# Optimization experiments

Measured on AMD Instinct MI355X. Metric: run time of the kernel, lower is better.

The kernel has to match this reference:

```python
import jax, jax.numpy as jnp
import numpy as np

H, D = 16, 64          # num_heads, head_dim
OUT = H * D            # out_dim = 1024
W1, W2 = 32, 32        # sliding windows
EPS_NORM = 1e-7
EPS_LN = 1e-5


def setup_inputs() -> dict:
    key = jax.random.key(0)
    ks = jax.random.split(key, 6)
    B, S, IN = 2, 2048, 1024
    x = jax.random.normal(ks[0], (B, S, IN), dtype=jnp.float32)
    scale = 0.02
    W_Q = jax.random.normal(ks[1], (IN, OUT), dtype=jnp.float32) * scale
    W_K = jax.random.normal(ks[2], (IN, OUT), dtype=jnp.float32) * scale
    W_V = jax.random.normal(ks[3], (IN, OUT), dtype=jnp.float32) * scale
    W_Kp = jax.random.normal(ks[4], (IN, OUT), dtype=jnp.float32) * scale
    W_O = jax.random.normal(ks[5], (OUT, OUT), dtype=jnp.float32) * scale
    ln_gamma = jnp.ones((OUT,), dtype=jnp.float32)
    ln_beta = jnp.zeros((OUT,), dtype=jnp.float32)
    return {"x": x, "W_Q": W_Q, "W_K": W_K, "W_V": W_V, "W_Kp": W_Kp,
            "W_O": W_O, "ln_gamma": ln_gamma, "ln_beta": ln_beta}


def _l2norm(t):
    return t / (jnp.linalg.norm(t, axis=-1, keepdims=True) + EPS_NORM)


def reference(x, W_Q, W_K, W_V, W_Kp, W_O, ln_gamma, ln_beta):
    B, S, _ = x.shape
    # projections -> (B, S, H, D)
    Q = _l2norm((x @ W_Q).reshape(B, S, H, D))
    K = _l2norm((x @ W_K).reshape(B, S, H, D))
    Kp = _l2norm((x @ W_Kp).reshape(B, S, H, D))
    V = (x @ W_V).reshape(B, S, H, D)
    # windowed keys/values (last w1/w2 positions, as in the PyTorch fallback)
    K_win = K[:, -W1:]
    Kp_win = Kp[:, -W2:]
    V_win = V[:, -W1:]
    Vp_win = V[:, -W2:]
    # triple product A_ijk = q.k.k' / sqrt(D) -> (B, S, H, w1, w2)
    A = jnp.einsum('bshd,bjhd,bkhd->bshjk', Q, K_win, Kp_win) / jnp.sqrt(jnp.float32(D))
    # causal window mask: allow j <= i + w1 - S and k <= i + w2 - S
    s_idx = jnp.arange(S)[:, None, None]
    j_idx = jnp.arange(W1)[None, :, None]
    k_idx = jnp.arange(W2)[None, None, :]
    mask = (j_idx > s_idx + (W1 - S)) | (k_idx > s_idx + (W2 - S))  # (S, w1, w2)
    neg_inf = jnp.float32(-jnp.inf)
    A = jnp.where(mask[None, :, None, :, :], neg_inf, A)
    # joint softmax over (j, k); fully-masked query rows produce zeros
    A_flat = A.reshape(B, S, H, W1 * W2)
    all_masked = jnp.all(A_flat == neg_inf, axis=-1, keepdims=True)
    A_safe = jnp.where(all_masked, 0.0, A_flat)
    P = jax.nn.softmax(A_safe, axis=-1)
    P = jnp.where(all_masked, 0.0, P).reshape(B, S, H, W1, W2)
    # value outer-product weighting (V' = V)
    Z = jnp.einsum('bshjk,bjhd,bkhd->bshd', P, V_win, Vp_win)
    out = Z.reshape(B, S, OUT) @ W_O
    out = out + x  # residual (shapes match)
    # LayerNorm
    mu = jnp.mean(out, axis=-1, keepdims=True)
    var = jnp.mean((out - mu) ** 2, axis=-1, keepdims=True)
    out = (out - mu) / jnp.sqrt(var + EPS_LN) * ln_gamma + ln_beta
    return out
```

## Files before the change

kernel.cpp:

```cpp
#include <hip/hip_runtime.h>
#include <math.h>


#define XS 68
#define WS 68
#define PS 36

#define YP_STR   262144
#define NKS_P    4
#define DP_OFF   (NKS_P * YP_STR)
#define DP_STR   65536

__device__ __forceinline__ void ln_row(
    const float4* __restrict__ x4, const float4* __restrict__ g4,
    const float4* __restrict__ b4, float4* __restrict__ out4,
    int row, int lane) {
  float4 v[4];
  #pragma unroll
  for (int i = 0; i < 4; i++) v[i] = x4[row * 256 + i * 64 + lane];
  float sum = 0.f, ss = 0.f;
  #pragma unroll
  for (int i = 0; i < 4; i++) {
    sum += v[i].x + v[i].y + v[i].z + v[i].w;
    ss  += v[i].x * v[i].x + v[i].y * v[i].y + v[i].z * v[i].z + v[i].w * v[i].w;
  }
  #pragma unroll
  for (int off = 1; off < 64; off <<= 1) {
    sum += __shfl_xor(sum, off);
    ss  += __shfl_xor(ss, off);
  }
  float mu   = sum * (1.f / 1024.f);
  float rstd = rsqrtf(ss * (1.f / 1024.f) - mu * mu + 1e-5f);
  #pragma unroll
  for (int i = 0; i < 4; i++) {
    float4 g  = g4[i * 64 + lane];
    float4 be = b4[i * 64 + lane];
    float4 o;
    o.x = (v[i].x - mu) * rstd * g.x + be.x;
    o.y = (v[i].y - mu) * rstd * g.y + be.y;
    o.z = (v[i].z - mu) * rstd * g.z + be.z;
    o.w = (v[i].w - mu) * rstd * g.w + be.w;
    out4[row * 256 + i * 64 + lane] = o;
  }
}

__global__ __launch_bounds__(256, 4) void proj_ln_kernel(
    const float* __restrict__ x,
    const float* __restrict__ Wq, const float* __restrict__ Wk,
    const float* __restrict__ Wkp, const float* __restrict__ Wv,
    const float* __restrict__ gam, const float* __restrict__ bet,
    float* __restrict__ Y, float* __restrict__ out) {
  __shared__ float xs[64 * WS];
  __shared__ float wl[64 * WS];
  const int tid = threadIdx.x;
  const int bid = blockIdx.x;

  if (bid < 256) {
    const int cb   = bid & 63;
    const int ks   = bid >> 6;
    const int col0 = cb * 64;
    const int z    = cb >> 4;
    const int colz = col0 & 1023;
    const float* __restrict__ W =
        (z == 0) ? Wq : ((z == 1) ? Wk : ((z == 2) ? Wkp : Wv));
    const int tc = tid & 15, tr = tid >> 4;

    float acc[4][4];
    #pragma unroll
    for (int i = 0; i < 4; i++)
      #pragma unroll
      for (int j = 0; j < 4; j++) acc[i][j] = 0.f;

    for (int cc = 0; cc < 4; cc++) {
      const int kb = ks * 256 + cc * 64;
      #pragma unroll
      for (int i = 0; i < 4; i++) {
        int e = i * 256 + tid;
        int r = e >> 4, q = e & 15;
        int b = r >> 5, t = r & 31;
        float4 v = *(const float4*)(x + ((b * 2048 + 2016 + t) * 1024 + kb + q * 4));
        xs[(q * 4 + 0) * WS + r] = v.x;
        xs[(q * 4 + 1) * WS + r] = v.y;
        xs[(q * 4 + 2) * WS + r] = v.z;
        xs[(q * 4 + 3) * WS + r] = v.w;
        float4 w = *(const float4*)(W + (size_t)(kb + r) * 1024 + colz + q * 4);
        *(float4*)(wl + r * WS + q * 4) = w;
      }
      __syncthreads();

      #pragma unroll 8
      for (int kk = 0; kk < 64; kk++) {
        float4 xv = *(const float4*)(xs + kk * WS + tr * 4);
        float4 wv = *(const float4*)(wl + kk * WS + tc * 4);
        acc[0][0] = fmaf(xv.x, wv.x, acc[0][0]);
        acc[0][1] = fmaf(xv.x, wv.y, acc[0][1]);
        acc[0][2] = fmaf(xv.x, wv.z, acc[0][2]);
        acc[0][3] = fmaf(xv.x, wv.w, acc[0][3]);
        acc[1][0] = fmaf(xv.y, wv.x, acc[1][0]);
        acc[1][1] = fmaf(xv.y, wv.y, acc[1][1]);
        acc[1][2] = fmaf(xv.y, wv.z, acc[1][2]);
        acc[1][3] = fmaf(xv.y, wv.w, acc[1][3]);
        acc[2][0] = fmaf(xv.z, wv.x, acc[2][0]);
        acc[2][1] = fmaf(xv.z, wv.y, acc[2][1]);
        acc[2][2] = fmaf(xv.z, wv.z, acc[2][2]);
        acc[2][3] = fmaf(xv.z, wv.w, acc[2][3]);
        acc[3][0] = fmaf(xv.w, wv.x, acc[3][0]);
        acc[3][1] = fmaf(xv.w, wv.y, acc[3][1]);
        acc[3][2] = fmaf(xv.w, wv.z, acc[3][2]);
        acc[3][3] = fmaf(xv.w, wv.w, acc[3][3]);
      }
      __syncthreads();
    }

    float* __restrict__ Yo = Y + ks * YP_STR + col0;
    #pragma unroll
    for (int i = 0; i < 4; i++) {
      float4 o = make_float4(acc[i][0], acc[i][1], acc[i][2], acc[i][3]);
      *(float4*)(Yo + (tr * 4 + i) * 4096 + tc * 4) = o;
    }
  } else {
    const int wave = tid >> 6, lane = tid & 63;
    const int gw = (bid - 256) * 4 + wave;
    const float4* x4 = (const float4*)x;
    const float4* g4 = (const float4*)gam;
    const float4* b4 = (const float4*)bet;
    float4* out4 = (float4*)out;
    for (int idx = gw; idx < 4032; idx += 1792) {
      int row = (idx < 2016) ? idx : idx + 32;
      ln_row(x4, g4, b4, out4, row, lane);
    }
  }
}

__global__ __launch_bounds__(256, 1) void attn_wo_kernel(
    const float* __restrict__ Yp, const float* __restrict__ Wo,
    float* __restrict__ Dp) {
  __shared__ float Kn[32 * XS], Kp[32 * XS], Vs[32 * XS];
  __shared__ float Pt[4][32 * PS];
  __shared__ float qs[4][64];
  __shared__ float Zs[4][64];
  const int tid = threadIdx.x;
  const int wave = tid >> 6, lane = tid & 63;
  const int bid = blockIdx.x;
  const int h = bid & 15, b = (bid >> 4) & 1, mb = bid >> 5;

  #pragma unroll
  for (int i = 0; i < 6; i++) {
    int e = i * 256 + tid;
    int a = e >> 9;
    int rem = e & 511;
    int row = rem >> 4, q = rem & 15;
    const float* src = Yp + (b * 32 + row) * 4096 + (a + 1) * 1024 + h * 64 + q * 4;
    float4 acc4 = make_float4(0.f, 0.f, 0.f, 0.f);
    #pragma unroll
    for (int p = 0; p < NKS_P; p++) {
      float4 v = *(const float4*)(src + p * YP_STR);
      acc4.x += v.x; acc4.y += v.y; acc4.z += v.z; acc4.w += v.w;
    }
    float* dst = (a == 0) ? Kn : ((a == 1) ? Kp : Vs);
    *(float4*)(dst + row * XS + q * 4) = acc4;
  }
  __syncthreads();

  for (int rr = 0; rr < 8; rr++) {
    int row = wave * 8 + rr;
    float kv = Kn[row * XS + lane];
    float s2 = kv * kv;
    #pragma unroll
    for (int off = 1; off < 64; off <<= 1) s2 += __shfl_xor(s2, off);
    Kn[row * XS + lane] = kv * (1.f / (sqrtf(s2) + 1e-7f));
    float pv = Kp[row * XS + lane];
    float p2 = pv * pv;
    #pragma unroll
    for (int off = 1; off < 64; off <<= 1) p2 += __shfl_xor(p2, off);
    Kp[row * XS + lane] = pv * (1.f / (sqrtf(p2) + 1e-7f));
  }
  __syncthreads();

  const int m = mb * 4 + wave;
  const int r = b * 32 + m;

  float q = 0.f;
  #pragma unroll
  for (int p = 0; p < NKS_P; p++)
    q += Yp[p * YP_STR + r * 4096 + h * 64 + lane];
  float q2 = q * q;
  #pragma unroll
  for (int off = 1; off < 64; off <<= 1) q2 += __shfl_xor(q2, off);
  q *= (1.f / (sqrtf(q2) + 1e-7f));
  qs[wave][lane] = q;
  __builtin_amdgcn_wave_barrier();

  const int lj = lane >> 3, lk = lane & 7;
  float acc[4][4];
  #pragma unroll
  for (int a = 0; a < 4; a++)
    #pragma unroll
    for (int c = 0; c < 4; c++) acc[a][c] = 0.f;

  const float* qw = qs[wave];
  for (int dq = 0; dq < 16; dq++) {
    float4 q4 = *(const float4*)(qw + dq * 4);
    float4 t4[4], kp4[4];
    #pragma unroll
    for (int tj = 0; tj < 4; tj++) {
      float4 kv = *(const float4*)(Kn + (lj * 4 + tj) * XS + dq * 4);
      t4[tj].x = q4.x * kv.x; t4[tj].y = q4.y * kv.y;
      t4[tj].z = q4.z * kv.z; t4[tj].w = q4.w * kv.w;
    }
    #pragma unroll
    for (int tk = 0; tk < 4; tk++)
      kp4[tk] = *(const float4*)(Kp + (lk * 4 + tk) * XS + dq * 4);
    #pragma unroll
    for (int tj = 0; tj < 4; tj++)
      #pragma unroll
      for (int tk = 0; tk < 4; tk++)
        acc[tj][tk] += t4[tj].x * kp4[tk].x + t4[tj].y * kp4[tk].y
                     + t4[tj].z * kp4[tk].z + t4[tj].w * kp4[tk].w;
  }

  float amax = -1e30f;
  #pragma unroll
  for (int tj = 0; tj < 4; tj++)
    #pragma unroll
    for (int tk = 0; tk < 4; tk++) {
      int j = lj * 4 + tj, k = lk * 4 + tk;
      if (j <= m && k <= m) amax = fmaxf(amax, acc[tj][tk] * 0.125f);
    }
  #pragma unroll
  for (int off = 1; off < 64; off <<= 1) amax = fmaxf(amax, __shfl_xor(amax, off));

  float lsum = 0.f;
  float* ptw = Pt[wave];
  #pragma unroll
  for (int tj = 0; tj < 4; tj++)
    #pragma unroll
    for (int tk = 0; tk < 4; tk++) {
      int j = lj * 4 + tj, k = lk * 4 + tk;
      float e = 0.f;
      if (j <= m && k <= m) e = __expf(acc[tj][tk] * 0.125f - amax);
      lsum += e;
      ptw[k * PS + j] = e;
    }
  #pragma unroll
  for (int off = 1; off < 64; off <<= 1) lsum += __shfl_xor(lsum, off);
  float inv = 1.f / lsum;
  __builtin_amdgcn_wave_barrier();

  float vreg[32];
  #pragma unroll
  for (int k = 0; k < 32; k++) vreg[k] = Vs[k * XS + lane];

  float zacc = 0.f;
  #pragma unroll
  for (int k = 0; k < 32; k++) {
    float g = 0.f;
    #pragma unroll
    for (int j4 = 0; j4 < 8; j4++) {
      float4 p4 = *(const float4*)(ptw + k * PS + j4 * 4);
      g += p4.x * vreg[j4 * 4 + 0] + p4.y * vreg[j4 * 4 + 1]
         + p4.z * vreg[j4 * 4 + 2] + p4.w * vreg[j4 * 4 + 3];
    }
    zacc = fmaf(g, vreg[k], zacc);
  }
  Zs[wave][lane] = zacc * inv;
  __syncthreads();

  float wacc[4][4];
  #pragma unroll
  for (int i = 0; i < 4; i++)
    #pragma unroll
    for (int j = 0; j < 4; j++) wacc[i][j] = 0.f;

  const float* __restrict__ WoS = Wo + (size_t)h * 65536 + tid * 4;
  #pragma unroll 4
  for (int k = 0; k < 64; k++) {
    float4 wv = *(const float4*)(WoS + (size_t)k * 1024);
    #pragma unroll
    for (int rr = 0; rr < 4; rr++) {
      float zz = Zs[rr][k];
      wacc[rr][0] = fmaf(zz, wv.x, wacc[rr][0]);
      wacc[rr][1] = fmaf(zz, wv.y, wacc[rr][1]);
      wacc[rr][2] = fmaf(zz, wv.z, wacc[rr][2]);
      wacc[rr][3] = fmaf(zz, wv.w, wacc[rr][3]);
    }
  }
  const int r0 = b * 32 + mb * 4;
  float* __restrict__ D = Dp + h * DP_STR;
  #pragma unroll
  for (int rr = 0; rr < 4; rr++) {
    float4 o = make_float4(wacc[rr][0], wacc[rr][1], wacc[rr][2], wacc[rr][3]);
    *(float4*)(D + (size_t)(r0 + rr) * 1024 + tid * 4) = o;
  }
}

__global__ __launch_bounds__(256, 4) void ln_win_kernel(
    const float4* __restrict__ x4, const float4* __restrict__ dp4,
    const float4* __restrict__ g4, const float4* __restrict__ b4,
    float4* __restrict__ out4) {
  __shared__ float red[8];
  const int tid = threadIdx.x;
  const int wave = tid >> 6, lane = tid & 63;
  const int wr  = blockIdx.x;
  const int row = (wr >> 5) * 2048 + 2016 + (wr & 31);

  float4 v = x4[row * 256 + tid];
  #pragma unroll
  for (int p = 0; p < 16; p++) {
    float4 d = dp4[p * 16384 + wr * 256 + tid];
    v.x += d.x; v.y += d.y; v.z += d.z; v.w += d.w;
  }
  float s  = v.x + v.y + v.z + v.w;
  float ss = v.x * v.x + v.y * v.y + v.z * v.z + v.w * v.w;
  #pragma unroll
  for (int off = 1; off < 64; off <<= 1) {
    s  += __shfl_xor(s, off);
    ss += __shfl_xor(ss, off);
  }
  if (lane == 0) { red[wave] = s; red[4 + wave] = ss; }
  __syncthreads();
  float sum = red[0] + red[1] + red[2] + red[3];
  float sq  = red[4] + red[5] + red[6] + red[7];
  float mu   = sum * (1.f / 1024.f);
  float rstd = rsqrtf(sq * (1.f / 1024.f) - mu * mu + 1e-5f);

  float4 g  = g4[tid];
  float4 be = b4[tid];
  float4 o;
  o.x = (v.x - mu) * rstd * g.x + be.x;
  o.y = (v.y - mu) * rstd * g.y + be.y;
  o.z = (v.z - mu) * rstd * g.z + be.z;
  o.w = (v.w - mu) * rstd * g.w + be.w;
  out4[row * 256 + tid] = o;
}

extern "C" void kernel_launch(void* const* d_in, const int* in_sizes, int n_in,
                              void* d_out, int out_size, void* d_ws, size_t ws_size,
                              hipStream_t stream) {
  const float* x   = (const float*)d_in[0];
  const float* Wq  = (const float*)d_in[1];
  const float* Wk  = (const float*)d_in[2];
  const float* Wv  = (const float*)d_in[3];
  const float* Wkp = (const float*)d_in[4];
  const float* Wo  = (const float*)d_in[5];
  const float* gam = (const float*)d_in[6];
  const float* bet = (const float*)d_in[7];
  float* out = (float*)d_out;
  float* ws  = (float*)d_ws;

  hipLaunchKernelGGL(proj_ln_kernel, dim3(256 + 448), dim3(256), 0, stream,
                     x, Wq, Wk, Wkp, Wv, gam, bet, ws, out);
  hipLaunchKernelGGL(attn_wo_kernel, dim3(256), dim3(256), 0, stream,
                     ws, Wo, ws + DP_OFF);
  hipLaunchKernelGGL(ln_win_kernel, dim3(64), dim3(256), 0, stream,
                     (const float4*)x, (const float4*)(ws + DP_OFF),
                     (const float4*)gam, (const float4*)bet, (float4*)out);
}
```

Measured before the change: 125.1 us.

## Register-prefetch next K-chunk in projection GEMM and store x tile row-major

```diff
diff --git a/kernel.cpp b/kernel.cpp
--- a/kernel.cpp
+++ b/kernel.cpp
@@ -44,7 +44,7 @@
   }
 }
 
-__global__ __launch_bounds__(256, 4) void proj_ln_kernel(
+__global__ __launch_bounds__(256, 3) void proj_ln_kernel(
     const float* __restrict__ x,
     const float* __restrict__ Wq, const float* __restrict__ Wk,
     const float* __restrict__ Wkp, const float* __restrict__ Wv,
@@ -65,49 +65,75 @@
         (z == 0) ? Wq : ((z == 1) ? Wk : ((z == 2) ? Wkp : Wv));
     const int tc = tid & 15, tr = tid >> 4;
 
+    const int er = tid >> 4;
+    const int eq = tid & 15;
+
     float acc[4][4];
     #pragma unroll
     for (int i = 0; i < 4; i++)
       #pragma unroll
       for (int j = 0; j < 4; j++) acc[i][j] = 0.f;
 
-    for (int cc = 0; cc < 4; cc++) {
-      const int kb = ks * 256 + cc * 64;
+    float4 px[4], pw[4];
+    {
+      const int kb = ks * 256;
       #pragma unroll
       for (int i = 0; i < 4; i++) {
-        int e = i * 256 + tid;
-        int r = e >> 4, q = e & 15;
-        int b = r >> 5, t = r & 31;
-        float4 v = *(const float4*)(x + ((b * 2048 + 2016 + t) * 1024 + kb + q * 4));
-        xs[(q * 4 + 0) * WS + r] = v.x;
-        xs[(q * 4 + 1) * WS + r] = v.y;
-        xs[(q * 4 + 2) * WS + r] = v.z;
-        xs[(q * 4 + 3) * WS + r] = v.w;
-        float4 w = *(const float4*)(W + (size_t)(kb + r) * 1024 + colz + q * 4);
-        *(float4*)(wl + r * WS + q * 4) = w;
+        int r = i * 16 + er;
+        int bb = r >> 5, t = r & 31;
+        px[i] = *(const float4*)(x + ((bb * 2048 + 2016 + t) * 1024 + kb + eq * 4));
+        pw[i] = *(const float4*)(W + (size_t)(kb + r) * 1024 + colz + eq * 4);
+      }
+    }
+
+    for (int cc = 0; cc < 4; cc++) {
+      #pragma unroll
+      for (int i = 0; i < 4; i++) {
+        int r = i * 16 + er;
+        *(float4*)(xs + r * WS + eq * 4) = px[i];
+        *(float4*)(wl + r * WS + eq * 4) = pw[i];
       }
       __syncthreads();
 
-      #pragma unroll 8
-      for (int kk = 0; kk < 64; kk++) {
-        float4 xv = *(const float4*)(xs + kk * WS + tr * 4);
-        float4 wv = *(const float4*)(wl + kk * WS + tc * 4);
-        acc[0][0] = fmaf(xv.x, wv.x, acc[0][0]);
-        acc[0][1] = fmaf(xv.x, wv.y, acc[0][1]);
-        acc[0][2] = fmaf(xv.x, wv.z, acc[0][2]);
-        acc[0][3] = fmaf(xv.x, wv.w, acc[0][3]);
-        acc[1][0] = fmaf(xv.y, wv.x, acc[1][0]);
-        acc[1][1] = fmaf(xv.y, wv.y, acc[1][1]);
-        acc[1][2] = fmaf(xv.y, wv.z, acc[1][2]);
-        acc[1][3] = fmaf(xv.y, wv.w, acc[1][3]);
-        acc[2][0] = fmaf(xv.z, wv.x, acc[2][0]);
-        acc[2][1] = fmaf(xv.z, wv.y, acc[2][1]);
-        acc[2][2] = fmaf(xv.z, wv.z, acc[2][2]);
-        acc[2][3] = fmaf(xv.z, wv.w, acc[2][3]);
-        acc[3][0] = fmaf(xv.w, wv.x, acc[3][0]);
-        acc[3][1] = fmaf(xv.w, wv.y, acc[3][1]);
-        acc[3][2] = fmaf(xv.w, wv.z, acc[3][2]);
-        acc[3][3] = fmaf(xv.w, wv.w, acc[3][3]);
+      if (cc < 3) {
+        const int kb = ks * 256 + (cc + 1) * 64;
+        #pragma unroll
+        for (int i = 0; i < 4; i++) {
+          int r = i * 16 + er;
+          int bb = r >> 5, t = r & 31;
+          px[i] = *(const float4*)(x + ((bb * 2048 + 2016 + t) * 1024 + kb + eq * 4));
+          pw[i] = *(const float4*)(W + (size_t)(kb + r) * 1024 + colz + eq * 4);
+        }
+      }
+
+      #pragma unroll 4
+      for (int kq = 0; kq < 16; kq++) {
+        float4 xr[4], wv[4];
+        #pragma unroll
+        for (int i = 0; i < 4; i++)
+          xr[i] = *(const float4*)(xs + (tr * 4 + i) * WS + kq * 4);
+        #pragma unroll
+        for (int s = 0; s < 4; s++)
+          wv[s] = *(const float4*)(wl + (kq * 4 + s) * WS + tc * 4);
+        #pragma unroll
+        for (int i = 0; i < 4; i++) {
+          acc[i][0] = fmaf(xr[i].x, wv[0].x, acc[i][0]);
+          acc[i][1] = fmaf(xr[i].x, wv[0].y, acc[i][1]);
+          acc[i][2] = fmaf(xr[i].x, wv[0].z, acc[i][2]);
+          acc[i][3] = fmaf(xr[i].x, wv[0].w, acc[i][3]);
+          acc[i][0] = fmaf(xr[i].y, wv[1].x, acc[i][0]);
+          acc[i][1] = fmaf(xr[i].y, wv[1].y, acc[i][1]);
+          acc[i][2] = fmaf(xr[i].y, wv[1].z, acc[i][2]);
+          acc[i][3] = fmaf(xr[i].y, wv[1].w, acc[i][3]);
+          acc[i][0] = fmaf(xr[i].z, wv[2].x, acc[i][0]);
+          acc[i][1] = fmaf(xr[i].z, wv[2].y, acc[i][1]);
+          acc[i][2] = fmaf(xr[i].z, wv[2].z, acc[i][2]);
+          acc[i][3] = fmaf(xr[i].z, wv[2].w, acc[i][3]);
+          acc[i][0] = fmaf(xr[i].w, wv[3].x, acc[i][0]);
+          acc[i][1] = fmaf(xr[i].w, wv[3].y, acc[i][1]);
+          acc[i][2] = fmaf(xr[i].w, wv[3].z, acc[i][2]);
+          acc[i][3] = fmaf(xr[i].w, wv[3].w, acc[i][3]);
+        }
       }
       __syncthreads();
     }
@@ -273,7 +299,7 @@
     for (int j = 0; j < 4; j++) wacc[i][j] = 0.f;
 
   const float* __restrict__ WoS = Wo + (size_t)h * 65536 + tid * 4;
-  #pragma unroll 4
+  #pragma unroll 8
   for (int k = 0; k < 64; k++) {
     float4 wv = *(const float4*)(WoS + (size_t)k * 1024);
     #pragma unroll
```

Result: slower. 135.2 us (+8.1%).
